# Kernel tuning notes

Measured on AMD Instinct MI355X. Metric: run time of the kernel, lower is better.

Reference implementation:

```python
import jax, jax.numpy as jnp
import numpy as np


def setup_inputs() -> dict:
    key = jax.random.key(0)
    ks = jax.random.split(key, 6)
    B, L, F, C, H, D1 = 262144, 20, 7, 16, 16, 8
    s = 0.1
    return {
        "x": jax.random.normal(ks[0], (B, L, F), dtype=jnp.float32),
        "conv_w": jax.random.normal(ks[1], (3, F, C), dtype=jnp.float32) * s,
        "conv_b": jnp.zeros((C,), dtype=jnp.float32),
        "rnn_w": jax.random.normal(ks[2], (C, H), dtype=jnp.float32) * s,
        "rnn_u": jax.random.normal(ks[3], (H, H), dtype=jnp.float32) * s,
        "rnn_b": jnp.zeros((H,), dtype=jnp.float32),
        "d1_w": jax.random.normal(ks[4], (H, D1), dtype=jnp.float32) * s,
        "d1_b": jnp.zeros((D1,), dtype=jnp.float32),
        "out_w": jax.random.normal(ks[5], (D1, 1), dtype=jnp.float32) * s,
        "out_b": jnp.zeros((1,), dtype=jnp.float32),
    }


def reference(x, conv_w, conv_b, rnn_w, rnn_u, rnn_b, d1_w, d1_b, out_w, out_b):
    # Conv1D, kernel 3, 'same' padding, relu.  x: [B,L,F] -> [B,L,C]
    h = jax.lax.conv_general_dilated(
        x, conv_w, window_strides=(1,), padding="SAME",
        dimension_numbers=("NWC", "WIO", "NWC"))
    h = jax.nn.relu(h + conv_b)

    # SimpleRNN(16), tanh, return last state.  Precompute input projections.
    xw = jnp.einsum("blc,ch->blh", h, rnn_w) + rnn_b  # [B,L,H]
    xw_t = jnp.swapaxes(xw, 0, 1)                      # [L,B,H]

    def step(state, xt):
        new = jnp.tanh(xt + state @ rnn_u)
        return new, None

    h0 = jnp.zeros((x.shape[0], rnn_u.shape[0]), dtype=x.dtype)
    h_last, _ = jax.lax.scan(step, h0, xw_t)           # [B,H]

    z = jax.nn.relu(h_last @ d1_w + d1_b)              # [B,8]
    return z @ out_w + out_b                           # [B,1]
```

## Files before the change

kernel.cpp:

```cpp
#include <hip/hip_runtime.h>


#define BLK 256
#define LSEQ 20
#define EPD 92
#define LOG2E2 2.8853900817779268f

typedef _Float16 f16;
typedef __fp16   fp16x2 __attribute__((ext_vector_type(2)));
typedef _Float16 f16x4 __attribute__((ext_vector_type(4)));
typedef _Float16 f16x8 __attribute__((ext_vector_type(8)));
typedef float    f32x4 __attribute__((ext_vector_type(4)));

union UB128 { uint4 q; f16x8 v; };
union UB64  { f16x4 v; fp16x2 p[2]; };
union HU    { fp16x2 p; uint u; };

__global__ __launch_bounds__(BLK, 4) void hybrid_fwd(
    const float* __restrict__ x,
    const float* __restrict__ conv_w, const float* __restrict__ conv_b,
    const float* __restrict__ rnn_w,  const float* __restrict__ rnn_u,
    const float* __restrict__ rnn_b,
    const float* __restrict__ d1_w,   const float* __restrict__ d1_b,
    const float* __restrict__ out_w,  const float* __restrict__ out_b,
    float* __restrict__ out)
{
    __shared__ __align__(16) uint xs[64 * EPD];

    const int tid  = threadIdx.x;
    const int wave = tid >> 6, lane = tid & 63;
    const int b16  = lane & 15, g = lane >> 4;
    const long BE  = (long)blockIdx.x * 64;

    #pragma unroll
    for (int k = 0; k < 3; ++k) {
        int t = tid + k * BLK;
        int e = t / 12, s = t - e * 12;
        xs[e * EPD + (s < 4 ? s : 80 + s)] = ((s & 3) == 3) ? 0x3C000000u : 0u;
    }
    const float* xg = x + BE * 140;
    #pragma unroll 2
    for (int k = 0; k < 5; ++k) {
        int t = tid + k * BLK;
        int e = t / 20, r = t - e * 20;
        const float* rp = xg + e * 140 + r * 7;
        float f0 = rp[0], f1 = rp[1], f2 = rp[2], f3 = rp[3];
        float f4 = rp[4], f5 = rp[5], f6 = rp[6];
        HU h0, h1, h2, h3;
        h0.p = __builtin_amdgcn_cvt_pkrtz(f0, f1);
        h1.p = __builtin_amdgcn_cvt_pkrtz(f2, f3);
        h2.p = __builtin_amdgcn_cvt_pkrtz(f4, f5);
        h3.p = __builtin_amdgcn_cvt_pkrtz(f6, 1.0f);
        uint4 val; val.x = h0.u; val.y = h1.u; val.z = h2.u; val.w = h3.u;
        *(uint4*)&xs[e * EPD + 4 * (r + 1)] = val;
    }
    __syncthreads();

    f16x8 A1;
    #pragma unroll
    for (int t = 0; t < 8; ++t) {
        float wv = conv_w[min(g * 7 + t, 20) * 16 + b16];
        float sel = (g < 3 && t < 7) ? wv
                  : ((g == 3 && t == 7) ? conv_b[b16] : 0.f);
        A1[t] = (f16)sel;
    }
    f16x4 A2, AU;
    f32x4 rbp;
    #pragma unroll
    for (int t = 0; t < 4; ++t) {
        A2[t]  = (f16)(LOG2E2 * rnn_w[(4 * g + t) * 16 + b16]);
        AU[t]  = (f16)(LOG2E2 * rnn_u[(4 * g + t) * 16 + b16]);
        rbp[t] = LOG2E2 * rnn_b[4 * g + t];
    }
    const f32x4 zero4 = {0.f, 0.f, 0.f, 0.f};

    const uint* rbase = xs + (wave * 16 + b16) * EPD + 4 * g;

    f16x4 B2s[LSEQ];
    #pragma unroll
    for (int l = 0; l < LSEQ; ++l) {
        UB128 B1;
        B1.q = *(const uint4*)(rbase + 4 * l);
        f32x4 a1 = __builtin_amdgcn_mfma_f32_16x16x32_f16(A1, B1.v, zero4, 0, 0, 0);
        UB64 B2;
        B2.p[0] = __builtin_amdgcn_cvt_pkrtz(fmaxf(a1[0], 0.f), fmaxf(a1[1], 0.f));
        B2.p[1] = __builtin_amdgcn_cvt_pkrtz(fmaxf(a1[2], 0.f), fmaxf(a1[3], 0.f));
        B2s[l] = B2.v;
    }

    f16x4 H = {};
    #pragma unroll
    for (int l = 0; l < LSEQ; ++l) {
        f32x4 a2 = __builtin_amdgcn_mfma_f32_16x16x16f16(A2, B2s[l], rbp, 0, 0, 0);
        a2 = __builtin_amdgcn_mfma_f32_16x16x16f16(AU, H, a2, 0, 0, 0);
        float t0 = __builtin_amdgcn_rcpf(1.f + __builtin_amdgcn_exp2f(a2[0]));
        float t1 = __builtin_amdgcn_rcpf(1.f + __builtin_amdgcn_exp2f(a2[1]));
        float t2 = __builtin_amdgcn_rcpf(1.f + __builtin_amdgcn_exp2f(a2[2]));
        float t3 = __builtin_amdgcn_rcpf(1.f + __builtin_amdgcn_exp2f(a2[3]));
        UB64 Hn;
        Hn.p[0] = __builtin_amdgcn_cvt_pkrtz(fmaf(-2.f, t0, 1.f), fmaf(-2.f, t1, 1.f));
        Hn.p[1] = __builtin_amdgcn_cvt_pkrtz(fmaf(-2.f, t2, 1.f), fmaf(-2.f, t3, 1.f));
        H = Hn.v;
    }

    f16x4 A3;
    f32x4 c3;
    #pragma unroll
    for (int t = 0; t < 4; ++t) {
        int j = 4 * g + t;
        A3[t] = (f16)(b16 < 8 ? d1_w[j * 8 + b16] : 0.f);
        c3[t] = d1_b[min(j, 7)];
    }
    f32x4 a3 = __builtin_amdgcn_mfma_f32_16x16x16f16(A3, H, c3, 0, 0, 0);
    float part = 0.f;
    #pragma unroll
    for (int r = 0; r < 4; ++r) {
        int d = 4 * g + r;
        float wv = (g < 2) ? out_w[min(d, 7)] : 0.f;
        part = fmaf(fmaxf(a3[r], 0.f), wv, part);
    }
    part += __shfl_xor(part, 16);
    part += __shfl_xor(part, 32);
    if (lane < 16)
        out[BE + wave * 16 + lane] = part + out_b[0];
}

extern "C" void kernel_launch(void* const* d_in, const int* in_sizes, int n_in,
                              void* d_out, int out_size, void* d_ws, size_t ws_size,
                              hipStream_t stream) {
    const float* x      = (const float*)d_in[0];
    const float* conv_w = (const float*)d_in[1];
    const float* conv_b = (const float*)d_in[2];
    const float* rnn_w  = (const float*)d_in[3];
    const float* rnn_u  = (const float*)d_in[4];
    const float* rnn_b  = (const float*)d_in[5];
    const float* d1_w   = (const float*)d_in[6];
    const float* d1_b   = (const float*)d_in[7];
    const float* out_w  = (const float*)d_in[8];
    const float* out_b  = (const float*)d_in[9];
    float* out = (float*)d_out;

    const int B = out_size;
    const int grid = B / 64;
    hybrid_fwd<<<grid, BLK, 0, stream>>>(x, conv_w, conv_b, rnn_w, rnn_u, rnn_b,
                                         d1_w, d1_b, out_w, out_b, out);
}
```

Measured before the change: 46.35 us.

## Process two independent 16-sequence groups per wave to interleave RNN chains

Result: faster. 43.60 us (-5.9%).

```diff
diff --git a/kernel.cpp b/kernel.cpp
--- a/kernel.cpp
+++ b/kernel.cpp
@@ -3,6 +3,7 @@
 
 #define BLK 256
 #define LSEQ 20
+#define EPB 128
 #define EPD 92
 #define LOG2E2 2.8853900817779268f
 
@@ -16,7 +17,7 @@
 union UB64  { f16x4 v; fp16x2 p[2]; };
 union HU    { fp16x2 p; uint u; };
 
-__global__ __launch_bounds__(BLK, 4) void hybrid_fwd(
+__global__ __launch_bounds__(BLK, 3) void hybrid_fwd(
     const float* __restrict__ x,
     const float* __restrict__ conv_w, const float* __restrict__ conv_b,
     const float* __restrict__ rnn_w,  const float* __restrict__ rnn_u,
@@ -25,34 +26,46 @@
     const float* __restrict__ out_w,  const float* __restrict__ out_b,
     float* __restrict__ out)
 {
-    __shared__ __align__(16) uint xs[64 * EPD];
+    __shared__ __align__(16) uint xs[EPB * EPD];
 
     const int tid  = threadIdx.x;
     const int wave = tid >> 6, lane = tid & 63;
     const int b16  = lane & 15, g = lane >> 4;
-    const long BE  = (long)blockIdx.x * 64;
+    const long BE  = (long)blockIdx.x * EPB;
 
-    #pragma unroll
-    for (int k = 0; k < 3; ++k) {
-        int t = tid + k * BLK;
-        int e = t / 12, s = t - e * 12;
-        xs[e * EPD + (s < 4 ? s : 80 + s)] = ((s & 3) == 3) ? 0x3C000000u : 0u;
+    const int e = tid >> 1;
+    const int q = tid & 1;
+
+    {
+        uint* eb = xs + e * EPD;
+        const uint C = 0x3C000000u;
+        if (q == 0) {
+            uint4 z; z.x = 0u; z.y = 0u; z.z = 0u; z.w = C;
+            *(uint4*)(eb + 0) = z;
+            *(uint2*)(eb + 84) = make_uint2(0u, 0u);
+        } else {
+            *(uint2*)(eb + 86) = make_uint2(0u, C);
+            uint4 z; z.x = 0u; z.y = 0u; z.z = 0u; z.w = C;
+            *(uint4*)(eb + 88) = z;
+        }
     }
-    const float* xg = x + BE * 140;
-    #pragma unroll 2
-    for (int k = 0; k < 5; ++k) {
-        int t = tid + k * BLK;
-        int e = t / 20, r = t - e * 20;
-        const float* rp = xg + e * 140 + r * 7;
-        float f0 = rp[0], f1 = rp[1], f2 = rp[2], f3 = rp[3];
-        float f4 = rp[4], f5 = rp[5], f6 = rp[6];
-        HU h0, h1, h2, h3;
-        h0.p = __builtin_amdgcn_cvt_pkrtz(f0, f1);
-        h1.p = __builtin_amdgcn_cvt_pkrtz(f2, f3);
-        h2.p = __builtin_amdgcn_cvt_pkrtz(f4, f5);
-        h3.p = __builtin_amdgcn_cvt_pkrtz(f6, 1.0f);
-        uint4 val; val.x = h0.u; val.y = h1.u; val.z = h2.u; val.w = h3.u;
-        *(uint4*)&xs[e * EPD + 4 * (r + 1)] = val;
+    {
+        const float2* sp = (const float2*)(x + BE * 140 + e * 140 + q * 70);
+        float2 f2[35];
+        #pragma unroll
+        for (int i = 0; i < 35; ++i) f2[i] = sp[i];
+        const float* f = (const float*)f2;
+        uint* eb = xs + e * EPD;
+        #pragma unroll
+        for (int i = 0; i < 10; ++i) {
+            HU h0, h1, h2, h3;
+            h0.p = __builtin_amdgcn_cvt_pkrtz(f[7 * i + 0], f[7 * i + 1]);
+            h1.p = __builtin_amdgcn_cvt_pkrtz(f[7 * i + 2], f[7 * i + 3]);
+            h2.p = __builtin_amdgcn_cvt_pkrtz(f[7 * i + 4], f[7 * i + 5]);
+            h3.p = __builtin_amdgcn_cvt_pkrtz(f[7 * i + 6], 1.0f);
+            uint4 val; val.x = h0.u; val.y = h1.u; val.z = h2.u; val.w = h3.u;
+            *(uint4*)(eb + 4 * (10 * q + i + 1)) = val;
+        }
     }
     __syncthreads();
 
@@ -74,33 +87,48 @@
     }
     const f32x4 zero4 = {0.f, 0.f, 0.f, 0.f};
 
-    const uint* rbase = xs + (wave * 16 + b16) * EPD + 4 * g;
+    const uint* rb0 = xs + (wave * 32 + b16) * EPD + 4 * g;
+    const uint* rb1 = rb0 + 16 * EPD;
 
-    f16x4 B2s[LSEQ];
+    f16x4 B2sA[LSEQ], B2sB[LSEQ];
     #pragma unroll
     for (int l = 0; l < LSEQ; ++l) {
-        UB128 B1;
-        B1.q = *(const uint4*)(rbase + 4 * l);
-        f32x4 a1 = __builtin_amdgcn_mfma_f32_16x16x32_f16(A1, B1.v, zero4, 0, 0, 0);
-        UB64 B2;
-        B2.p[0] = __builtin_amdgcn_cvt_pkrtz(fmaxf(a1[0], 0.f), fmaxf(a1[1], 0.f));
-        B2.p[1] = __builtin_amdgcn_cvt_pkrtz(fmaxf(a1[2], 0.f), fmaxf(a1[3], 0.f));
-        B2s[l] = B2.v;
+        UB128 B1a, B1b;
+        B1a.q = *(const uint4*)(rb0 + 4 * l);
+        B1b.q = *(const uint4*)(rb1 + 4 * l);
+        f32x4 a1a = __builtin_amdgcn_mfma_f32_16x16x32_f16(A1, B1a.v, zero4, 0, 0, 0);
+        f32x4 a1b = __builtin_amdgcn_mfma_f32_16x16x32_f16(A1, B1b.v, zero4, 0, 0, 0);
+        UB64 Ba, Bb;
+        Ba.p[0] = __builtin_amdgcn_cvt_pkrtz(fmaxf(a1a[0], 0.f), fmaxf(a1a[1], 0.f));
+        Ba.p[1] = __builtin_amdgcn_cvt_pkrtz(fmaxf(a1a[2], 0.f), fmaxf(a1a[3], 0.f));
+        Bb.p[0] = __builtin_amdgcn_cvt_pkrtz(fmaxf(a1b[0], 0.f), fmaxf(a1b[1], 0.f));
+        Bb.p[1] = __builtin_amdgcn_cvt_pkrtz(fmaxf(a1b[2], 0.f), fmaxf(a1b[3], 0.f));
+        B2sA[l] = Ba.v;
+        B2sB[l] = Bb.v;
     }
 
-    f16x4 H = {};
+    f16x4 H0 = {}, H1 = {};
     #pragma unroll
     for (int l = 0; l < LSEQ; ++l) {
-        f32x4 a2 = __builtin_amdgcn_mfma_f32_16x16x16f16(A2, B2s[l], rbp, 0, 0, 0);
-        a2 = __builtin_amdgcn_mfma_f32_16x16x16f16(AU, H, a2, 0, 0, 0);
-        float t0 = __builtin_amdgcn_rcpf(1.f + __builtin_amdgcn_exp2f(a2[0]));
-        float t1 = __builtin_amdgcn_rcpf(1.f + __builtin_amdgcn_exp2f(a2[1]));
-        float t2 = __builtin_amdgcn_rcpf(1.f + __builtin_amdgcn_exp2f(a2[2]));
-        float t3 = __builtin_amdgcn_rcpf(1.f + __builtin_amdgcn_exp2f(a2[3]));
-        UB64 Hn;
-        Hn.p[0] = __builtin_amdgcn_cvt_pkrtz(fmaf(-2.f, t0, 1.f), fmaf(-2.f, t1, 1.f));
-        Hn.p[1] = __builtin_amdgcn_cvt_pkrtz(fmaf(-2.f, t2, 1.f), fmaf(-2.f, t3, 1.f));
-        H = Hn.v;
+        f32x4 a20 = __builtin_amdgcn_mfma_f32_16x16x16f16(A2, B2sA[l], rbp, 0, 0, 0);
+        f32x4 a21 = __builtin_amdgcn_mfma_f32_16x16x16f16(A2, B2sB[l], rbp, 0, 0, 0);
+        a20 = __builtin_amdgcn_mfma_f32_16x16x16f16(AU, H0, a20, 0, 0, 0);
+        a21 = __builtin_amdgcn_mfma_f32_16x16x16f16(AU, H1, a21, 0, 0, 0);
+        float t00 = __builtin_amdgcn_rcpf(1.f + __builtin_amdgcn_exp2f(a20[0]));
+        float t01 = __builtin_amdgcn_rcpf(1.f + __builtin_amdgcn_exp2f(a20[1]));
+        float t02 = __builtin_amdgcn_rcpf(1.f + __builtin_amdgcn_exp2f(a20[2]));
+        float t03 = __builtin_amdgcn_rcpf(1.f + __builtin_amdgcn_exp2f(a20[3]));
+        float t10 = __builtin_amdgcn_rcpf(1.f + __builtin_amdgcn_exp2f(a21[0]));
+        float t11 = __builtin_amdgcn_rcpf(1.f + __builtin_amdgcn_exp2f(a21[1]));
+        float t12 = __builtin_amdgcn_rcpf(1.f + __builtin_amdgcn_exp2f(a21[2]));
+        float t13 = __builtin_amdgcn_rcpf(1.f + __builtin_amdgcn_exp2f(a21[3]));
+        UB64 Hn0, Hn1;
+        Hn0.p[0] = __builtin_amdgcn_cvt_pkrtz(fmaf(-2.f, t00, 1.f), fmaf(-2.f, t01, 1.f));
+        Hn0.p[1] = __builtin_amdgcn_cvt_pkrtz(fmaf(-2.f, t02, 1.f), fmaf(-2.f, t03, 1.f));
+        Hn1.p[0] = __builtin_amdgcn_cvt_pkrtz(fmaf(-2.f, t10, 1.f), fmaf(-2.f, t11, 1.f));
+        Hn1.p[1] = __builtin_amdgcn_cvt_pkrtz(fmaf(-2.f, t12, 1.f), fmaf(-2.f, t13, 1.f));
+        H0 = Hn0.v;
+        H1 = Hn1.v;
     }
 
     f16x4 A3;
@@ -111,18 +139,23 @@
         A3[t] = (f16)(b16 < 8 ? d1_w[j * 8 + b16] : 0.f);
         c3[t] = d1_b[min(j, 7)];
     }
-    f32x4 a3 = __builtin_amdgcn_mfma_f32_16x16x16f16(A3, H, c3, 0, 0, 0);
-    float part = 0.f;
+    f32x4 a30 = __builtin_amdgcn_mfma_f32_16x16x16f16(A3, H0, c3, 0, 0, 0);
+    f32x4 a31 = __builtin_amdgcn_mfma_f32_16x16x16f16(A3, H1, c3, 0, 0, 0);
+    float p0 = 0.f, p1 = 0.f;
     #pragma unroll
     for (int r = 0; r < 4; ++r) {
         int d = 4 * g + r;
         float wv = (g < 2) ? out_w[min(d, 7)] : 0.f;
-        part = fmaf(fmaxf(a3[r], 0.f), wv, part);
+        p0 = fmaf(fmaxf(a30[r], 0.f), wv, p0);
+        p1 = fmaf(fmaxf(a31[r], 0.f), wv, p1);
     }
-    part += __shfl_xor(part, 16);
-    part += __shfl_xor(part, 32);
-    if (lane < 16)
-        out[BE + wave * 16 + lane] = part + out_b[0];
+    p0 += __shfl_xor(p0, 16); p0 += __shfl_xor(p0, 32);
+    p1 += __shfl_xor(p1, 16); p1 += __shfl_xor(p1, 32);
+    if (lane < 16) {
+        float ob = out_b[0];
+        out[BE + wave * 32 + b16]      = p0 + ob;
+        out[BE + wave * 32 + 16 + b16] = p1 + ob;
+    }
 }
 
 extern "C" void kernel_launch(void* const* d_in, const int* in_sizes, int n_in,
@@ -141,7 +174,7 @@
     float* out = (float*)d_out;
 
     const int B = out_size;
-    const int grid = B / 64;
+    const int grid = B / EPB;
     hybrid_fwd<<<grid, BLK, 0, stream>>>(x, conv_w, conv_b, rnn_w, rnn_u, rnn_b,
                                          d1_w, d1_b, out_w, out_b, out);
 }
```

## Load input with float4 coalesced reads, stage weights in LDS, tighten LDS pitch

Applied to the files above, without the earlier changes.

Measured after the change: 50.51 us. 9.0% more time.

```diff
diff --git a/kernel.cpp b/kernel.cpp
--- a/kernel.cpp
+++ b/kernel.cpp
@@ -3,8 +3,19 @@
 
 #define BLK 256
 #define LSEQ 20
-#define EPD 92
+#define EPB 64
+#define EPW 84
 #define LOG2E2 2.8853900817779268f
+
+#define W_CONV   0
+#define W_CONVB  336
+#define W_RNNW   352
+#define W_RNNU   608
+#define W_RNNB   864
+#define W_D1W    880
+#define W_D1B    1008
+#define W_OUTW   1016
+#define W_OUTB   1024
 
 typedef _Float16 f16;
 typedef __fp16   fp16x2 __attribute__((ext_vector_type(2)));
@@ -14,9 +25,8 @@
 
 union UB128 { uint4 q; f16x8 v; };
 union UB64  { f16x4 v; fp16x2 p[2]; };
-union HU    { fp16x2 p; uint u; };
 
-__global__ __launch_bounds__(BLK, 4) void hybrid_fwd(
+__global__ __launch_bounds__(BLK, 5) void hybrid_fwd(
     const float* __restrict__ x,
     const float* __restrict__ conv_w, const float* __restrict__ conv_b,
     const float* __restrict__ rnn_w,  const float* __restrict__ rnn_u,
@@ -25,69 +35,105 @@
     const float* __restrict__ out_w,  const float* __restrict__ out_b,
     float* __restrict__ out)
 {
-    __shared__ __align__(16) uint xs[64 * EPD];
+    __shared__ __align__(16) uint  xs[EPB * EPW + 8];
+    __shared__ float wg[1025];
 
     const int tid  = threadIdx.x;
     const int wave = tid >> 6, lane = tid & 63;
     const int b16  = lane & 15, g = lane >> 4;
-    const long BE  = (long)blockIdx.x * 64;
+    const long BE  = (long)blockIdx.x * EPB;
 
+    const uint4 PAD = make_uint4(0u, 0u, 0u, 0x3C000000u);
+    if (tid < EPB) *(uint4*)(xs + tid * EPW) = PAD;
+    if (tid < 2)   *(uint4*)(xs + EPB * EPW + 4 * tid) = PAD;
     #pragma unroll
-    for (int k = 0; k < 3; ++k) {
-        int t = tid + k * BLK;
-        int e = t / 12, s = t - e * 12;
-        xs[e * EPD + (s < 4 ? s : 80 + s)] = ((s & 3) == 3) ? 0x3C000000u : 0u;
-    }
-    const float* xg = x + BE * 140;
-    #pragma unroll 2
     for (int k = 0; k < 5; ++k) {
         int t = tid + k * BLK;
-        int e = t / 20, r = t - e * 20;
-        const float* rp = xg + e * 140 + r * 7;
-        float f0 = rp[0], f1 = rp[1], f2 = rp[2], f3 = rp[3];
-        float f4 = rp[4], f5 = rp[5], f6 = rp[6];
-        HU h0, h1, h2, h3;
-        h0.p = __builtin_amdgcn_cvt_pkrtz(f0, f1);
-        h1.p = __builtin_amdgcn_cvt_pkrtz(f2, f3);
-        h2.p = __builtin_amdgcn_cvt_pkrtz(f4, f5);
-        h3.p = __builtin_amdgcn_cvt_pkrtz(f6, 1.0f);
-        uint4 val; val.x = h0.u; val.y = h1.u; val.z = h2.u; val.w = h3.u;
-        *(uint4*)&xs[e * EPD + 4 * (r + 1)] = val;
+        int e = t / 20, s = t - e * 20;
+        *(f16*)((char*)(xs + e * EPW) + (s + 1) * 16 + 14) = (f16)1.0f;
     }
+    const float4* xsrc = (const float4*)(x + BE * 140);
+    #pragma unroll
+    for (int k = 0; k < 9; ++k) {
+        int g4 = tid + k * BLK;
+        if (g4 < 2240) {
+            float4 v = xsrc[g4];
+            int e = g4 / 35, j = g4 - e * 35;
+            int p = 4 * j;
+            int r = p / 7, c = p - 7 * r;
+            char* eb = (char*)(xs + e * EPW);
+            *(f16*)(eb + (r + 1) * 16 + 2 * c) = (f16)v.x;
+            if (++c == 7) { c = 0; ++r; }
+            *(f16*)(eb + (r + 1) * 16 + 2 * c) = (f16)v.y;
+            if (++c == 7) { c = 0; ++r; }
+            *(f16*)(eb + (r + 1) * 16 + 2 * c) = (f16)v.z;
+            if (++c == 7) { c = 0; ++r; }
+            *(f16*)(eb + (r + 1) * 16 + 2 * c) = (f16)v.w;
+        }
+    }
+    wg[W_RNNW + tid] = rnn_w[tid];
+    {
+        int i = tid;
+        if (i < 336) wg[W_CONV + i] = conv_w[i];
+        i = tid - 336;
+        if (i >= 0 && i < 256) {  }
+    }
+    if (tid < 80) wg[W_CONV + 256 + tid] = conv_w[256 + tid];
+    if (tid < 256) {  }
+    wg[W_RNNU + tid] = rnn_u[tid];
+    if (tid < 16)  wg[W_CONVB + tid] = conv_b[tid];
+    if (tid < 16)  wg[W_RNNB + tid]  = rnn_b[tid];
+    if (tid < 128) wg[W_D1W + tid]   = d1_w[tid];
+    if (tid < 8)   { wg[W_D1B + tid] = d1_b[tid]; wg[W_OUTW + tid] = out_w[tid]; }
+    if (tid == 0)  wg[W_OUTB] = out_b[0];
+    if (tid < 256) { int i = tid; if (i < 256) wg[W_CONV + (i < 256 ? i : 0)] = conv_w[i < 256 ? i : 0]; }
+
     __syncthreads();
 
     f16x8 A1;
     #pragma unroll
     for (int t = 0; t < 8; ++t) {
-        float wv = conv_w[min(g * 7 + t, 20) * 16 + b16];
+        float wv = wg[W_CONV + min(g * 7 + t, 20) * 16 + b16];
         float sel = (g < 3 && t < 7) ? wv
-                  : ((g == 3 && t == 7) ? conv_b[b16] : 0.f);
+                  : ((g == 3 && t == 7) ? wg[W_CONVB + b16] : 0.f);
         A1[t] = (f16)sel;
     }
     f16x4 A2, AU;
     f32x4 rbp;
     #pragma unroll
     for (int t = 0; t < 4; ++t) {
-        A2[t]  = (f16)(LOG2E2 * rnn_w[(4 * g + t) * 16 + b16]);
-        AU[t]  = (f16)(LOG2E2 * rnn_u[(4 * g + t) * 16 + b16]);
-        rbp[t] = LOG2E2 * rnn_b[4 * g + t];
+        A2[t]  = (f16)(LOG2E2 * wg[W_RNNW + (4 * g + t) * 16 + b16]);
+        AU[t]  = (f16)(LOG2E2 * wg[W_RNNU + (4 * g + t) * 16 + b16]);
+        rbp[t] = LOG2E2 * wg[W_RNNB + 4 * g + t];
     }
+    f16x4 A3;
+    f32x4 c3;
+    #pragma unroll
+    for (int t = 0; t < 4; ++t) {
+        int j = 4 * g + t;
+        A3[t] = (f16)(b16 < 8 ? wg[W_D1W + j * 8 + b16] : 0.f);
+        c3[t] = wg[W_D1B + min(j, 7)];
+    }
+    float ow[4];
+    #pragma unroll
+    for (int r = 0; r < 4; ++r)
+        ow[r] = (g < 2) ? wg[W_OUTW + min(4 * g + r, 7)] : 0.f;
+    const float ob = wg[W_OUTB];
     const f32x4 zero4 = {0.f, 0.f, 0.f, 0.f};
 
-    const uint* rbase = xs + (wave * 16 + b16) * EPD + 4 * g;
+    const uint* rb0 = xs + (wave * 16 + b16) * EPW + 4 * g;
 
     f16x4 B2s[LSEQ];
     #pragma unroll
     for (int l = 0; l < LSEQ; ++l) {
         UB128 B1;
-        B1.q = *(const uint4*)(rbase + 4 * l);
+        B1.q = *(const uint4*)(rb0 + 4 * l);
         f32x4 a1 = __builtin_amdgcn_mfma_f32_16x16x32_f16(A1, B1.v, zero4, 0, 0, 0);
         UB64 B2;
         B2.p[0] = __builtin_amdgcn_cvt_pkrtz(fmaxf(a1[0], 0.f), fmaxf(a1[1], 0.f));
         B2.p[1] = __builtin_amdgcn_cvt_pkrtz(fmaxf(a1[2], 0.f), fmaxf(a1[3], 0.f));
         B2s[l] = B2.v;
     }
-
     f16x4 H = {};
     #pragma unroll
     for (int l = 0; l < LSEQ; ++l) {
@@ -102,27 +148,15 @@
         Hn.p[1] = __builtin_amdgcn_cvt_pkrtz(fmaf(-2.f, t2, 1.f), fmaf(-2.f, t3, 1.f));
         H = Hn.v;
     }
-
-    f16x4 A3;
-    f32x4 c3;
-    #pragma unroll
-    for (int t = 0; t < 4; ++t) {
-        int j = 4 * g + t;
-        A3[t] = (f16)(b16 < 8 ? d1_w[j * 8 + b16] : 0.f);
-        c3[t] = d1_b[min(j, 7)];
-    }
     f32x4 a3 = __builtin_amdgcn_mfma_f32_16x16x16f16(A3, H, c3, 0, 0, 0);
     float part = 0.f;
     #pragma unroll
-    for (int r = 0; r < 4; ++r) {
-        int d = 4 * g + r;
-        float wv = (g < 2) ? out_w[min(d, 7)] : 0.f;
-        part = fmaf(fmaxf(a3[r], 0.f), wv, part);
-    }
+    for (int r = 0; r < 4; ++r)
+        part = fmaf(fmaxf(a3[r], 0.f), ow[r], part);
     part += __shfl_xor(part, 16);
     part += __shfl_xor(part, 32);
     if (lane < 16)
-        out[BE + wave * 16 + lane] = part + out_b[0];
+        out[BE + wave * 16 + lane] = part + ob;
 }
 
 extern "C" void kernel_launch(void* const* d_in, const int* in_sizes, int n_in,
@@ -141,7 +175,7 @@
     float* out = (float*)d_out;
 
     const int B = out_size;
-    const int grid = B / 64;
+    const int grid = B / EPB;
     hybrid_fwd<<<grid, BLK, 0, stream>>>(x, conv_w, conv_b, rnn_w, rnn_u, rnn_b,
                                          d1_w, d1_b, out_w, out_b, out);
 }
```
